# Kernel tuning notes

Hardware: AMD Instinct MI355X
Metric: run time of the kernel (lower is better)

Reference implementation:

```python
import jax, jax.numpy as jnp
from jax import lax
import numpy as np

T_NO = 50       # history / kernel half-length (hard-coded in module)
T_MAX = 101     # basis kernel length = 2*T_NO + 1
BASIS_NO = 34
HIST_BASIS_NO = 18
SIGMA = 3.0
HID = 20
SUB = 20


def _make_basis(n_basis, length):
    # basis[i, t] = exp(-(t - 3*i)^2 / sigma)
    raw = jnp.arange(length, dtype=jnp.float32)
    pts = 3.0 * jnp.arange(n_basis, dtype=jnp.float32)
    return jnp.exp(-((raw[None, :] - pts[:, None]) ** 2) / SIGMA)


def _conv1d(x, kern, pad):
    # x: [1, Cin, T], kern: [Cout, Cin, K] -> [1, Cout, T'] (torch F.conv1d semantics, cross-correlation)
    return lax.conv_general_dilated(x, kern, window_strides=(1,), padding=[(pad, pad)],
                                    dimension_numbers=('NCH', 'OIH', 'NCH'))


def setup_inputs() -> dict:
    key = jax.random.key(0)
    ks = jax.random.split(key, 12)
    T, Ee, Ei = 200000, 500, 100
    S_e = (jax.random.uniform(ks[0], (T, Ee)) < 0.05).astype(jnp.float32)
    S_i = (jax.random.uniform(ks[1], (T, Ei)) < 0.05).astype(jnp.float32)
    # one-hot synapse->subunit connectivity, as in the original model
    C_syn_e = jax.nn.one_hot(jax.random.randint(ks[2], (Ee,), 0, SUB), SUB, dtype=jnp.float32).T
    C_syn_i = jax.nn.one_hot(jax.random.randint(ks[3], (Ei,), 0, SUB), SUB, dtype=jnp.float32).T
    weight1 = 0.01 * jax.random.normal(ks[4], (HID, 2 * SUB, BASIS_NO), dtype=jnp.float32)
    weight4 = 0.01 * jax.random.normal(ks[5], (1, HID, BASIS_NO), dtype=jnp.float32)
    W_hist = 0.01 * jax.random.normal(ks[6], (HIST_BASIS_NO,), dtype=jnp.float32)
    Theta = 0.01 * jax.random.normal(ks[7], (1,), dtype=jnp.float32)
    W_spk = jnp.ones((1,), jnp.float32)
    Tau_spk = 3.0 * jnp.ones((1,), jnp.float32)
    u = jax.random.uniform(ks[8], (T,), dtype=jnp.float32)  # bernoulli noise
    return dict(S_e=S_e, S_i=S_i, C_syn_e=C_syn_e, C_syn_i=C_syn_i,
                weight1=weight1, weight4=weight4, W_hist=W_hist, Theta=Theta,
                W_spk=W_spk, Tau_spk=Tau_spk, u=u)


def reference(S_e, S_i, C_syn_e, C_syn_i, weight1, weight4, W_hist, Theta, W_spk, Tau_spk, u):
    basis = _make_basis(BASIS_NO, T_MAX)          # [34, 101]
    hist_basis = _make_basis(HIST_BASIS_NO, T_NO)  # [18, 50]

    kern1 = jnp.einsum('hsb,bt->hst', weight1, basis)  # [HID, 2*SUB, 101]
    kern4 = jnp.einsum('ohb,bt->oht', weight4, basis)  # [1, HID, 101]

    # route synapses to subunits, stack e/i: [1, 2*SUB, T]
    syn_in = jnp.concatenate([S_e @ C_syn_e.T, S_i @ C_syn_i.T], axis=1).T[None]
    out1 = jax.nn.leaky_relu(_conv1d(syn_in, kern1, T_NO), 0.01)  # [1, HID, T]
    out4 = _conv1d(out1, kern4, T_NO)[0, 0]                        # [T]

    hist_kern = W_hist @ hist_basis  # [50]
    theta = Theta[0]

    def step(buf, inp):
        # buf: last T_NO spikes, oldest first (== spk_out[t:t+T_NO])
        o_t, u_t = inp
        p = jax.nn.sigmoid(o_t + buf @ hist_kern + theta)
        spk = (u_t < p).astype(jnp.float32)  # torch.bernoulli(p)
        buf = jnp.concatenate([buf[1:], spk[None]])
        return buf, (p, spk)

    buf0 = jnp.zeros((T_NO,), jnp.float32)
    _, (prob_out, spikes) = lax.scan(step, buf0, (out4, u))
    spk_out = jnp.concatenate([jnp.zeros((T_NO,), jnp.float32), spikes])  # [T + T_NO]

    t = jnp.arange(T_NO, dtype=jnp.float32)
    t_tau = t / (Tau_spk[0] ** 2)
    spk_kern = t_tau * jnp.exp(-t_tau) * (W_spk[0] ** 2)  # unflipped; torch flips then cross-correlates
    # torch conv1d(x, flip(k), valid) == jnp.convolve(x, k, 'valid')
    spk_filt = jnp.convolve(spk_out, spk_kern, mode='valid')[:-1]  # [T]
    return (spk_filt, prob_out)
```

## Files before the change

kernel.cpp:

```cpp
#include <hip/hip_runtime.h>
#include <math.h>

#define T_TOT  200000
#define EE     500
#define EI     100
#define SUBN   20
#define NCH    40
#define HIDN   20
#define BNO    34
#define TM     101
#define TNO    50
#define HBNO   18
#define TT1    256
#define EPSF   2e-5f
#define NTAP   58

#define PADL   64
#define PADR   256
#define SROW   (PADL + T_TOT + PADR)

#define GROW   (T_TOT + 112)

#define GW     355
#define SW     380

#define RTILE  512
#define RHALO  64
#define RRND   3
#define NTILE  ((T_TOT + 1023) / 1024)

__global__ void k_setup(const float* __restrict__ Ce, const float* __restrict__ Ci,
                        const float* __restrict__ Wh, const float* __restrict__ Wspk,
                        const float* __restrict__ Tau,
                        int* __restrict__ ae, int* __restrict__ ai,
                        float* __restrict__ hkpos, float* __restrict__ hkneg,
                        float* __restrict__ spkk, float* __restrict__ gtap,
                        double* __restrict__ hkd, double* __restrict__ basisd)
{
    int tid = threadIdx.x;
    if (tid < EE) {
        int a = 0;
        for (int s = 0; s < SUBN; ++s) if (Ce[s * EE + tid] > 0.5f) a = s;
        ae[tid] = a;
    } else if (tid < EE + EI) {
        int e = tid - EE; int a = 0;
        for (int s = 0; s < SUBN; ++s) if (Ci[s * EI + e] > 0.5f) a = s;
        ai[e] = a;
    } else if (tid < 664) {
        int j = tid - 600;
        double hk = 0.0;
        if (j >= 1 && j <= TNO) {
            int i = TNO - j;
            for (int b = 0; b < HBNO; ++b) {
                double d = (double)i - 3.0 * (double)b;
                hk += (double)Wh[b] * exp(-d * d / 3.0);
            }
        }
        hkd[j] = hk;
        hkpos[j] = (float)fmax(hk, 0.0);
        hkneg[j] = (float)fmin(hk, 0.0);
    } else if (tid < 728) {
        int m = tid - 664; float v = 0.f;
        if (m < TNO) {
            double tau2 = (double)Tau[0] * (double)Tau[0];
            double tt = (double)m / tau2;
            v = (float)(tt * exp(-tt) * (double)Wspk[0] * (double)Wspk[0]);
        }
        spkk[m] = v;
    } else if (tid < 753) {
        int j = tid - 740;
        gtap[tid - 728] = (float)exp(-(double)(j * j) / 3.0);
    }
    for (int idx = tid; idx < BNO * TM; idx += blockDim.x) {
        int b = idx / TM, k = idx % TM;
        double d = (double)k - 3.0 * (double)b;
        basisd[idx] = exp(-d * d / 3.0);
    }
}

__global__ void k_prep(const float* __restrict__ w1, const float* __restrict__ w4,
                       const double* __restrict__ basisd,
                       float* __restrict__ kern4, float* __restrict__ cmerged,
                       float* __restrict__ syn)
{
    int idx = blockIdx.x * 256 + threadIdx.x;
    if (idx < HIDN * TM) {
        int h = idx % HIDN, k = idx / HIDN;
        double acc = 0.0;
        for (int b = 0; b < BNO; ++b) acc += (double)w4[h * BNO + b] * basisd[b * TM + k];
        kern4[k * HIDN + h] = (float)acc;
    } else if (idx < 2020 + NCH * NTAP * HIDN) {
        int j = idx - 2020;
        int h = j % HIDN, tap = (j / HIDN) % NTAP, s = j / (HIDN * NTAP);
        float val;
        if (tap < BNO) {
            val = w1[(h * NCH + s) * BNO + tap];
        } else {
            int mi = tap - BNO;
            int m = (mi < 12) ? (mi - 62) : (mi + 39);
            double acc = 0.0;
            for (int b = 0; b < BNO; ++b) {
                int jj = m + 50 - 3 * b;
                if (jj >= -12 && jj <= 12)
                    acc += (double)w1[(h * NCH + s) * BNO + b] * exp(-(double)(jj * jj) / 3.0);
            }
            val = -(float)acc;
        }
        cmerged[j] = val;
    } else if (idx < 2020 + NCH * NTAP * HIDN + NCH * (PADL + PADR)) {
        int j = idx - (2020 + NCH * NTAP * HIDN);
        int r = j / (PADL + PADR), c = j % (PADL + PADR);
        int off = (c < PADL) ? c : (PADL + T_TOT + (c - PADL));
        syn[(size_t)r * SROW + off] = 0.f;
    }
}

__global__ __launch_bounds__(256) void k_route(const float* __restrict__ Se,
                                               const float* __restrict__ Si,
                                               const int* __restrict__ ae,
                                               const int* __restrict__ ai,
                                               float* __restrict__ syn)
{
    __shared__ float acc[NCH * 64];
    __shared__ int sae[EE];
    __shared__ int sai[EI];
    int tid = threadIdx.x;
    for (int i = tid; i < NCH * 64; i += 256) acc[i] = 0.f;
    for (int i = tid; i < EE; i += 256) sae[i] = ae[i];
    for (int i = tid; i < EI; i += 256) sai[i] = ai[i];
    __syncthreads();
    int t0 = blockIdx.x * 64;
    int lane = tid & 63, grp = tid >> 6;
    for (int ec = 0; ec < 2; ++ec) {
        int ev = ec * 64 + lane;
        if (ev < EE / 4) {
            int e = 4 * ev;
            int a0 = sae[e], a1 = sae[e + 1], a2 = sae[e + 2], a3 = sae[e + 3];
            for (int ts = grp; ts < 64; ts += 8) {
                float4 v1 = *(const float4*)(Se + (size_t)(t0 + ts) * EE + e);
                float4 v2 = *(const float4*)(Se + (size_t)(t0 + ts + 4) * EE + e);
                if (v1.x != 0.f) atomicAdd(&acc[a0 * 64 + ts], v1.x);
                if (v1.y != 0.f) atomicAdd(&acc[a1 * 64 + ts], v1.y);
                if (v1.z != 0.f) atomicAdd(&acc[a2 * 64 + ts], v1.z);
                if (v1.w != 0.f) atomicAdd(&acc[a3 * 64 + ts], v1.w);
                if (v2.x != 0.f) atomicAdd(&acc[a0 * 64 + ts + 4], v2.x);
                if (v2.y != 0.f) atomicAdd(&acc[a1 * 64 + ts + 4], v2.y);
                if (v2.z != 0.f) atomicAdd(&acc[a2 * 64 + ts + 4], v2.z);
                if (v2.w != 0.f) atomicAdd(&acc[a3 * 64 + ts + 4], v2.w);
            }
        }
    }
    {
        int ev = lane;
        if (ev < EI / 4) {
            int e = 4 * ev;
            int a0 = sai[e] + SUBN, a1 = sai[e + 1] + SUBN, a2 = sai[e + 2] + SUBN, a3 = sai[e + 3] + SUBN;
            for (int ts = grp; ts < 64; ts += 8) {
                float4 v1 = *(const float4*)(Si + (size_t)(t0 + ts) * EI + e);
                float4 v2 = *(const float4*)(Si + (size_t)(t0 + ts + 4) * EI + e);
                if (v1.x != 0.f) atomicAdd(&acc[a0 * 64 + ts], v1.x);
                if (v1.y != 0.f) atomicAdd(&acc[a1 * 64 + ts], v1.y);
                if (v1.z != 0.f) atomicAdd(&acc[a2 * 64 + ts], v1.z);
                if (v1.w != 0.f) atomicAdd(&acc[a3 * 64 + ts], v1.w);
                if (v2.x != 0.f) atomicAdd(&acc[a0 * 64 + ts + 4], v2.x);
                if (v2.y != 0.f) atomicAdd(&acc[a1 * 64 + ts + 4], v2.y);
                if (v2.z != 0.f) atomicAdd(&acc[a2 * 64 + ts + 4], v2.z);
                if (v2.w != 0.f) atomicAdd(&acc[a3 * 64 + ts + 4], v2.w);
            }
        }
    }
    __syncthreads();
    for (int i = tid; i < NCH * 64; i += 256) {
        int s = i >> 6, ts = i & 63;
        syn[(size_t)s * SROW + PADL + t0 + ts] = acc[i];
    }
}

__global__ __launch_bounds__(256) void k_prefilt(const float* __restrict__ syn,
                                                 const float* __restrict__ gtap,
                                                 float* __restrict__ G)
{
    int gi = blockIdx.x * 256 + threadIdx.x;
    if (gi >= GROW) return;
    const float* sp = syn + (size_t)blockIdx.y * SROW + PADL + (gi - 50);
    double a = 0.0;
#pragma unroll
    for (int j = -12; j <= 12; ++j)
        a += (double)gtap[j + 12] * (double)sp[j];
    G[(size_t)blockIdx.y * GROW + gi] = (float)a;
}

__global__ __launch_bounds__(256) void k_conv1h(const float* __restrict__ G,
                                                const float* __restrict__ syn,
                                                const float* __restrict__ cmerged,
                                                float* __restrict__ out1)
{
    __shared__ float sg[2][GW];
    __shared__ float ss[2][SW];
    __shared__ float sc[2][NTAP * HIDN];
    int tid = threadIdx.x;
    int t0 = blockIdx.x * 256;
    int t = t0 + tid;

    {
        const float* Gp = G + t0;
        const float* sp = syn + PADL + t0 - 62;
        for (int i = tid; i < GW; i += 256)
            sg[0][i] = (t0 + i < GROW) ? Gp[i] : 0.f;
        for (int i = tid; i < SW; i += 256)
            ss[0][i] = sp[i];
        for (int i = tid; i < NTAP * HIDN; i += 256)
            sc[0][i] = cmerged[i];
    }

    float acc[HIDN];
#pragma unroll
    for (int h = 0; h < HIDN; ++h) acc[h] = 0.f;

    for (int s = 0; s < NCH; ++s) {
        __syncthreads();
        int cb = s & 1, nb = cb ^ 1;
        if (s + 1 < NCH) {
            const float* Gp = G + (size_t)(s + 1) * GROW + t0;
            const float* sp = syn + (size_t)(s + 1) * SROW + PADL + t0 - 62;
            const float* cp = cmerged + (size_t)(s + 1) * (NTAP * HIDN);
            for (int i = tid; i < GW; i += 256)
                sg[nb][i] = (t0 + i < GROW) ? Gp[i] : 0.f;
            for (int i = tid; i < SW; i += 256)
                ss[nb][i] = sp[i];
            for (int i = tid; i < NTAP * HIDN; i += 256)
                sc[nb][i] = cp[i];
        }
        const float* sgc = sg[cb];
        const float* ssc = ss[cb];
        const float* cc = sc[cb];
#pragma unroll 2
        for (int b = 0; b < BNO; ++b) {
            float gv = sgc[tid + 3 * b];
            const float4* cp4 = (const float4*)(cc + b * HIDN);
#pragma unroll
            for (int q = 0; q < 5; ++q) {
                float4 c = cp4[q];
                acc[4 * q + 0] = fmaf(c.x, gv, acc[4 * q + 0]);
                acc[4 * q + 1] = fmaf(c.y, gv, acc[4 * q + 1]);
                acc[4 * q + 2] = fmaf(c.z, gv, acc[4 * q + 2]);
                acc[4 * q + 3] = fmaf(c.w, gv, acc[4 * q + 3]);
            }
        }
#pragma unroll 2
        for (int mi = 0; mi < 12; ++mi) {
            float xv = ssc[tid + mi];
            const float4* cp4 = (const float4*)(cc + (BNO + mi) * HIDN);
#pragma unroll
            for (int q = 0; q < 5; ++q) {
                float4 c = cp4[q];
                acc[4 * q + 0] = fmaf(c.x, xv, acc[4 * q + 0]);
                acc[4 * q + 1] = fmaf(c.y, xv, acc[4 * q + 1]);
                acc[4 * q + 2] = fmaf(c.z, xv, acc[4 * q + 2]);
                acc[4 * q + 3] = fmaf(c.w, xv, acc[4 * q + 3]);
            }
        }
#pragma unroll 2
        for (int mi = 12; mi < 24; ++mi) {
            float xv = ssc[tid + mi + 101];
            const float4* cp4 = (const float4*)(cc + (BNO + mi) * HIDN);
#pragma unroll
            for (int q = 0; q < 5; ++q) {
                float4 c = cp4[q];
                acc[4 * q + 0] = fmaf(c.x, xv, acc[4 * q + 0]);
                acc[4 * q + 1] = fmaf(c.y, xv, acc[4 * q + 1]);
                acc[4 * q + 2] = fmaf(c.z, xv, acc[4 * q + 2]);
                acc[4 * q + 3] = fmaf(c.w, xv, acc[4 * q + 3]);
            }
        }
    }
    if (t < T_TOT) {
#pragma unroll
        for (int h = 0; h < HIDN; ++h) {
            float o = acc[h];
            out1[(size_t)h * T_TOT + t] = (o > 0.f) ? o : 0.01f * o;
        }
    }
}

__global__ __launch_bounds__(256) void k_conv2(const float* __restrict__ out1,
                                               const float* __restrict__ kern4,
                                               const float* __restrict__ Theta,
                                               const float* __restrict__ u,
                                               double* __restrict__ xd,
                                               double* __restrict__ thrd,
                                               float* __restrict__ thr32,
                                               float* __restrict__ blo,
                                               float* __restrict__ bhi)
{
    __shared__ float s1[HIDN * (TT1 + 100)];
    int tid = threadIdx.x;
    int t0 = blockIdx.x * TT1;
    for (int i = tid; i < HIDN * (TT1 + 100); i += 256) {
        int h = i / (TT1 + 100), x = i % (TT1 + 100);
        int g = t0 + x - TNO;
        s1[i] = (g >= 0 && g < T_TOT) ? out1[(size_t)h * T_TOT + g] : 0.f;
    }
    __syncthreads();
    int t = t0 + tid;
    if (t >= T_TOT) return;
    double acc = 0.0;
    for (int k = 0; k < TM; ++k) {
        const float* kp = kern4 + k * HIDN;
#pragma unroll
        for (int h = 0; h < HIDN; ++h)
            acc = fma((double)s1[h * (TT1 + 100) + tid + k], (double)kp[h], acc);
    }
    double x = acc + (double)Theta[0];
    double uu = (double)u[t];
    double th = (log(uu) - log1p(-uu)) - x;
    xd[t] = x; thrd[t] = th; thr32[t] = (float)th;
    blo[t + TNO] = 0.f;
    bhi[t + TNO] = 1.f;
    if (t < TNO) { blo[t] = 0.f; bhi[t] = 0.f; }
    if (t < 14)  { blo[T_TOT + TNO + t] = 0.f; bhi[T_TOT + TNO + t] = 0.f; }
}

__global__ __launch_bounds__(256) void k_relax(const float* __restrict__ thr32,
                                               const float* __restrict__ hkpos,
                                               const float* __restrict__ hkneg,
                                               float* __restrict__ blo,
                                               float* __restrict__ bhi)
{
    __shared__ float slo[RTILE + RHALO], shi[RTILE + RHALO];
    __shared__ float sth[RTILE + RHALO];
    __shared__ float shp[64], shn[64];
    int tid = threadIdx.x;
    int t0 = blockIdx.x * RTILE;
    for (int i = tid; i < RTILE + RHALO; i += 256) {
        int t = t0 - RHALO + i;
        int g = t + TNO;
        bool ok = (g >= 0 && g < T_TOT + 64);
        slo[i] = ok ? blo[g] : 0.f;
        shi[i] = ok ? bhi[g] : 0.f;
        sth[i] = (t >= 0 && t < T_TOT) ? thr32[t] : 0.f;
    }
    if (tid < 64) { shp[tid] = hkpos[tid]; shn[tid] = hkneg[tid]; }
    __syncthreads();
    for (int r = 0; r < RRND; ++r) {
        for (int i = tid; i < RTILE + RHALO; i += 256) {
            if (i < TNO) continue;
            float l = slo[i], h = shi[i];
            if (l == h) continue;
            float lo = 0.f, hi = 0.f;
            for (int j = 1; j <= TNO; ++j) {
                float bl = slo[i - j], bh = shi[i - j];
                float hp = shp[j], hn = shn[j];
                lo = fmaf(hp, bl, lo); lo = fmaf(hn, bh, lo);
                hi = fmaf(hp, bh, hi); hi = fmaf(hn, bl, hi);
            }
            float th = sth[i];
            if (lo > th + EPSF)      slo[i] = 1.f;
            else if (hi < th - EPSF) shi[i] = 0.f;
        }
        __syncthreads();
    }
    for (int i = tid; i < RTILE; i += 256) {
        int t = t0 + i;
        if (t < T_TOT) {
            blo[t + TNO] = slo[RHALO + i];
            bhi[t + TNO] = shi[RHALO + i];
        }
    }
}

__global__ __launch_bounds__(1024) void k_mark(const float* __restrict__ blo,
                                               const float* __restrict__ bhi,
                                               int* __restrict__ dirty)
{
    int t = blockIdx.x * 1024 + threadIdx.x;
    int unk = (t < T_TOT) && (blo[t + TNO] != bhi[t + TNO]);
    int c = __syncthreads_count(unk);
    if (threadIdx.x == 0) dirty[blockIdx.x] = c;
}

__global__ __launch_bounds__(1024) void k_compact(const float* __restrict__ blo,
                                                  const float* __restrict__ bhi,
                                                  const int* __restrict__ dirty,
                                                  int* __restrict__ list,
                                                  int* __restrict__ utot)
{
    __shared__ int wsum[16];
    __shared__ int sd[NTILE];
    __shared__ int sbase;
    int tid = threadIdx.x;
    if (tid < NTILE) sd[tid] = dirty[tid];
    int t = blockIdx.x * 1024 + tid;
    int unk = (t < T_TOT) && (blo[t + TNO] != bhi[t + TNO]);
    unsigned long long m = __ballot(unk);
    int lane = tid & 63, wv = tid >> 6;
    int lr = __popcll(m & ((1ull << lane) - 1ull));
    if (lane == 0) wsum[wv] = __popcll(m);
    __syncthreads();
    if (tid == 0) {
        int b = 0;
        for (int k = 0; k < (int)blockIdx.x; ++k) b += sd[k];
        sbase = b;
        if (blockIdx.x == 0) {
            int tot = 0;
            for (int k = 0; k < NTILE; ++k) tot += sd[k];
            utot[0] = tot;
        }
        int r = 0;
        for (int k = 0; k < 16; ++k) { int c = wsum[k]; wsum[k] = r; r += c; }
    }
    __syncthreads();
    if (unk) list[sbase + wsum[wv] + lr] = t;
}

__global__ __launch_bounds__(256) void k_afix(const int* __restrict__ list,
                                              const int* __restrict__ utot,
                                              const float* __restrict__ blo,
                                              const double* __restrict__ hkd,
                                              double* __restrict__ afix)
{
    int i = blockIdx.x * 256 + threadIdx.x;
    if (i >= utot[0]) return;
    int t = list[i];
    double a = 0.0;
    for (int j = 1; j <= TNO; ++j)
        a += hkd[j] * (double)blo[t - j + TNO];
    afix[i] = a;
}

__global__ __launch_bounds__(256) void k_chain(const int* __restrict__ list,
                                               int* __restrict__ utot,
                                               int* __restrict__ chead)
{
    __shared__ int wcnt[4];
    __shared__ int base_s;
    int tid = threadIdx.x, lane = tid & 63, wv = tid >> 6;
    int U = utot[0];
    if (tid == 0) base_s = 0;
    __syncthreads();
    for (int b0 = 0; b0 < U; b0 += 256) {
        int i = b0 + tid;
        int head = 0;
        if (i < U) head = (i == 0) || (list[i] - list[i - 1] > TNO);
        unsigned long long m = __ballot(head);
        int pre = __popcll(m & ((1ull << lane) - 1ull));
        if (lane == 0) wcnt[wv] = __popcll(m);
        __syncthreads();
        int wbase = 0;
        for (int k = 0; k < wv; ++k) wbase += wcnt[k];
        int tot = wcnt[0] + wcnt[1] + wcnt[2] + wcnt[3];
        if (head) chead[base_s + wbase + pre] = i;
        __syncthreads();
        if (tid == 0) base_s += tot;
        __syncthreads();
    }
    if (tid == 0) utot[1] = base_s;
}

__global__ __launch_bounds__(256) void k_cresolve(const int* __restrict__ list,
                                                  const int* __restrict__ chead,
                                                  const double* __restrict__ afix,
                                                  const double* __restrict__ thrd,
                                                  const double* __restrict__ hkd,
                                                  const int* __restrict__ utot,
                                                  int* bits,
                                                  float* __restrict__ blo,
                                                  float* __restrict__ bhi)
{
    __shared__ double shk[64];
    if (threadIdx.x < 64)
        shk[threadIdx.x] = (threadIdx.x >= 1 && threadIdx.x <= TNO) ? hkd[threadIdx.x] : 0.0;
    __syncthreads();
    int c = blockIdx.x * 256 + threadIdx.x;
    int nch = utot[1];
    if (c >= nch) return;
    int i0 = chead[c];
    int i1 = (c + 1 < nch) ? chead[c + 1] : utot[0];
    for (int i = i0; i < i1; ++i) {
        int t = list[i];
        double a = afix[i];
        for (int k = i - 1; k >= i0; --k) {
            int dt = t - list[k];
            if (dt > TNO) break;
            if (bits[k]) a += shk[dt];
        }
        int sb = (a > thrd[t]) ? 1 : 0;
        bits[i] = sb;
        float f = (float)sb;
        blo[t + TNO] = f;
        bhi[t + TNO] = f;
    }
}

__global__ __launch_bounds__(256) void k_out(const float* __restrict__ blo,
                                             const float* __restrict__ spkk,
                                             const double* __restrict__ hkd,
                                             const double* __restrict__ xd,
                                             float* __restrict__ outp)
{
    __shared__ float sb[TT1 + 64];
    __shared__ float ssp[64];
    __shared__ double shk[64];
    int tid = threadIdx.x;
    int t0 = blockIdx.x * TT1;
    for (int i = tid; i < TT1 + TNO; i += 256) {
        int g = t0 + i;
        sb[i] = (g < T_TOT + 64) ? blo[g] : 0.f;
    }
    if (tid < 64) { ssp[tid] = spkk[tid]; shk[tid] = hkd[tid]; }
    __syncthreads();
    int t = t0 + tid;
    if (t >= T_TOT) return;
    float filt = 0.f;
    double a = 0.0;
    for (int m = 1; m <= TNO; ++m) {
        float b = sb[tid + TNO - m];
        filt = fmaf(b, ssp[m - 1], filt);
        a += shk[m] * (double)b;
    }
    double p = 1.0 / (1.0 + exp(-(xd[t] + a)));
    outp[t] = filt;
    outp[T_TOT + t] = (float)p;
}

extern "C" void kernel_launch(void* const* d_in, const int* in_sizes, int n_in,
                              void* d_out, int out_size, void* d_ws, size_t ws_size,
                              hipStream_t stream)
{
    (void)in_sizes; (void)n_in; (void)out_size; (void)ws_size;
    const float* Se = (const float*)d_in[0];
    const float* Si = (const float*)d_in[1];
    const float* Ce = (const float*)d_in[2];
    const float* Ci = (const float*)d_in[3];
    const float* w1 = (const float*)d_in[4];
    const float* w4 = (const float*)d_in[5];
    const float* Wh = (const float*)d_in[6];
    const float* Th = (const float*)d_in[7];
    const float* Ws = (const float*)d_in[8];
    const float* Ta = (const float*)d_in[9];
    const float* u  = (const float*)d_in[10];

    char* w = (char*)d_ws;
    size_t off = 0;
    auto alloc = [&](size_t n) { size_t o = off; off += (n + 15) & ~(size_t)15; return o; };

    size_t gzone = alloc((size_t)NCH * GROW * 4);
    float*  G     = (float*)(w + gzone);
    double* xd    = (double*)(w + gzone);
    double* thrd  = (double*)(w + gzone + 1600000);
    float*  thr32 = (float*)(w + gzone + 3200000);
    float*  blo   = (float*)(w + gzone + 4000000);
    float*  bhi   = (float*)(w + gzone + 4800512);
    int*    dirty = (int*)(w + gzone + 5600768);
    int*    list  = (int*)(w + gzone + 5601792);
    double* afix  = (double*)(w + gzone + 6401792);
    int*    chead = (int*)(w + gzone + 8001792);
    int*    bits  = (int*)(w + gzone + 8801800);
    int*    utot  = dirty + 200;

    float*  syn     = (float*)(w + alloc((size_t)NCH * SROW * 4));
    float*  out1    = (float*)(w + alloc((size_t)HIDN * T_TOT * 4));
    float*  kern4   = (float*)(w + alloc((size_t)TM * HIDN * 4));
    float*  cmerged = (float*)(w + alloc((size_t)NCH * NTAP * HIDN * 4));
    double* basisd  = (double*)(w + alloc((size_t)BNO * TM * 8));
    int*    ae      = (int*)(w + alloc(EE * 4));
    int*    ai      = (int*)(w + alloc(EI * 4));
    float*  hkpos   = (float*)(w + alloc(64 * 4));
    float*  hkneg   = (float*)(w + alloc(64 * 4));
    float*  spkk    = (float*)(w + alloc(64 * 4));
    float*  gtap    = (float*)(w + alloc(32 * 4));
    double* hkd     = (double*)(w + alloc(64 * 8));

    k_setup<<<1, 1024, 0, stream>>>(Ce, Ci, Wh, Ws, Ta, ae, ai, hkpos, hkneg, spkk, gtap, hkd, basisd);
    int prepN = 2020 + NCH * NTAP * HIDN + NCH * (PADL + PADR);
    k_prep<<<(prepN + 255) / 256, 256, 0, stream>>>(w1, w4, basisd, kern4, cmerged, syn);
    k_route<<<T_TOT / 64, 256, 0, stream>>>(Se, Si, ae, ai, syn);
    dim3 pg((GROW + 255) / 256, NCH);
    k_prefilt<<<pg, 256, 0, stream>>>(syn, gtap, G);
    k_conv1h<<<(T_TOT + 255) / 256, 256, 0, stream>>>(G, syn, cmerged, out1);
    k_conv2<<<(T_TOT + TT1 - 1) / TT1, 256, 0, stream>>>(out1, kern4, Th, u, xd, thrd, thr32, blo, bhi);
    for (int r = 0; r < 4; ++r)
        k_relax<<<(T_TOT + RTILE - 1) / RTILE, 256, 0, stream>>>(thr32, hkpos, hkneg, blo, bhi);
    k_mark<<<NTILE, 1024, 0, stream>>>(blo, bhi, dirty);
    k_compact<<<NTILE, 1024, 0, stream>>>(blo, bhi, dirty, list, utot);
    k_chain<<<1, 256, 0, stream>>>(list, utot, chead);
    k_afix<<<(T_TOT + 255) / 256, 256, 0, stream>>>(list, utot, blo, hkd, afix);
    k_cresolve<<<(T_TOT + 255) / 256, 256, 0, stream>>>(list, chead, afix, thrd, hkd, utot, bits, blo, bhi);
    k_out<<<(T_TOT + TT1 - 1) / TT1, 256, 0, stream>>>(blo, spkk, hkd, xd, (float*)d_out);
}
```

Measured before the change: 1.195 ms.

## Register-block conv1 over two timesteps per thread and fuse dirty marking into relax

The first conv kernel now has each wave handle half of the hidden channels while each thread computes two adjacent timesteps. This halves the shared-memory coefficient loads per FMA, and the coefficients are repacked into a padded layout of 12 floats per tap. The relax pass count drops from four launches to two, with more rounds inside each launch. The separate mark kernel is replaced by a dirty-count written from the final relax. Compaction now uses 512-wide tiles to match, which cuts launches, but fewer relaxation passes may leave more unresolved timesteps for the later fixup stages.

```diff
diff --git a/kernel.cpp b/kernel.cpp
--- a/kernel.cpp
+++ b/kernel.cpp
@@ -14,6 +14,7 @@
 #define TT1    256
 #define EPSF   2e-5f
 #define NTAP   58
+#define CPT    12
 
 #define PADL   64
 #define PADR   256
@@ -23,11 +24,12 @@
 
 #define GW     355
 #define SW     380
+#define CW     (2 * NTAP * CPT)
 
 #define RTILE  512
 #define RHALO  64
-#define RRND   3
-#define NTILE  ((T_TOT + 1023) / 1024)
+#define RRND   4
+#define NT2    ((T_TOT + RTILE - 1) / RTILE)
 
 __global__ void k_setup(const float* __restrict__ Ce, const float* __restrict__ Ci,
                         const float* __restrict__ Wh, const float* __restrict__ Wspk,
@@ -89,26 +91,29 @@
         double acc = 0.0;
         for (int b = 0; b < BNO; ++b) acc += (double)w4[h * BNO + b] * basisd[b * TM + k];
         kern4[k * HIDN + h] = (float)acc;
-    } else if (idx < 2020 + NCH * NTAP * HIDN) {
+    } else if (idx < 2020 + NCH * CW) {
         int j = idx - 2020;
-        int h = j % HIDN, tap = (j / HIDN) % NTAP, s = j / (HIDN * NTAP);
-        float val;
-        if (tap < BNO) {
-            val = w1[(h * NCH + s) * BNO + tap];
-        } else {
-            int mi = tap - BNO;
-            int m = (mi < 12) ? (mi - 62) : (mi + 39);
-            double acc = 0.0;
-            for (int b = 0; b < BNO; ++b) {
-                int jj = m + 50 - 3 * b;
-                if (jj >= -12 && jj <= 12)
-                    acc += (double)w1[(h * NCH + s) * BNO + b] * exp(-(double)(jj * jj) / 3.0);
+        int f = j % CPT, tap = (j / CPT) % NTAP, hg = (j / (CPT * NTAP)) & 1, s = j / CW;
+        float val = 0.f;
+        if (f < 10) {
+            int h = hg * 10 + f;
+            if (tap < BNO) {
+                val = w1[(h * NCH + s) * BNO + tap];
+            } else {
+                int mi = tap - BNO;
+                int m = (mi < 12) ? (mi - 62) : (mi + 39);
+                double acc = 0.0;
+                for (int b = 0; b < BNO; ++b) {
+                    int jj = m + 50 - 3 * b;
+                    if (jj >= -12 && jj <= 12)
+                        acc += (double)w1[(h * NCH + s) * BNO + b] * exp(-(double)(jj * jj) / 3.0);
+                }
+                val = -(float)acc;
             }
-            val = -(float)acc;
         }
         cmerged[j] = val;
-    } else if (idx < 2020 + NCH * NTAP * HIDN + NCH * (PADL + PADR)) {
-        int j = idx - (2020 + NCH * NTAP * HIDN);
+    } else if (idx < 2020 + NCH * CW + NCH * (PADL + PADR)) {
+        int j = idx - (2020 + NCH * CW);
         int r = j / (PADL + PADR), c = j % (PADL + PADR);
         int off = (c < PADL) ? c : (PADL + T_TOT + (c - PADL));
         syn[(size_t)r * SROW + off] = 0.f;
@@ -190,32 +195,43 @@
     G[(size_t)blockIdx.y * GROW + gi] = (float)a;
 }
 
-__global__ __launch_bounds__(256) void k_conv1h(const float* __restrict__ G,
+#define FMA10(c0, c1, c2, v0, v1)                                              \
+    acc[0][0] = fmaf(c0.x, v0, acc[0][0]); acc[0][1] = fmaf(c0.x, v1, acc[0][1]); \
+    acc[1][0] = fmaf(c0.y, v0, acc[1][0]); acc[1][1] = fmaf(c0.y, v1, acc[1][1]); \
+    acc[2][0] = fmaf(c0.z, v0, acc[2][0]); acc[2][1] = fmaf(c0.z, v1, acc[2][1]); \
+    acc[3][0] = fmaf(c0.w, v0, acc[3][0]); acc[3][1] = fmaf(c0.w, v1, acc[3][1]); \
+    acc[4][0] = fmaf(c1.x, v0, acc[4][0]); acc[4][1] = fmaf(c1.x, v1, acc[4][1]); \
+    acc[5][0] = fmaf(c1.y, v0, acc[5][0]); acc[5][1] = fmaf(c1.y, v1, acc[5][1]); \
+    acc[6][0] = fmaf(c1.z, v0, acc[6][0]); acc[6][1] = fmaf(c1.z, v1, acc[6][1]); \
+    acc[7][0] = fmaf(c1.w, v0, acc[7][0]); acc[7][1] = fmaf(c1.w, v1, acc[7][1]); \
+    acc[8][0] = fmaf(c2.x, v0, acc[8][0]); acc[8][1] = fmaf(c2.x, v1, acc[8][1]); \
+    acc[9][0] = fmaf(c2.y, v0, acc[9][0]); acc[9][1] = fmaf(c2.y, v1, acc[9][1]);
+
+__global__ __launch_bounds__(256) void k_conv1w(const float* __restrict__ G,
                                                 const float* __restrict__ syn,
                                                 const float* __restrict__ cmerged,
                                                 float* __restrict__ out1)
 {
     __shared__ float sg[2][GW];
     __shared__ float ss[2][SW];
-    __shared__ float sc[2][NTAP * HIDN];
-    int tid = threadIdx.x;
+    __shared__ float sc[2][CW];
+    int tid = threadIdx.x;
+    int wv = tid >> 6, lane = tid & 63;
+    int hg = wv & 1, tsub = wv >> 1;
+    int tloc = tsub * 128 + lane * 2;
     int t0 = blockIdx.x * 256;
-    int t = t0 + tid;
 
     {
         const float* Gp = G + t0;
         const float* sp = syn + PADL + t0 - 62;
-        for (int i = tid; i < GW; i += 256)
-            sg[0][i] = (t0 + i < GROW) ? Gp[i] : 0.f;
-        for (int i = tid; i < SW; i += 256)
-            ss[0][i] = sp[i];
-        for (int i = tid; i < NTAP * HIDN; i += 256)
-            sc[0][i] = cmerged[i];
-    }
-
-    float acc[HIDN];
+        for (int i = tid; i < GW; i += 256) sg[0][i] = (t0 + i < GROW) ? Gp[i] : 0.f;
+        for (int i = tid; i < SW; i += 256) ss[0][i] = sp[i];
+        for (int i = tid; i < CW; i += 256) sc[0][i] = cmerged[i];
+    }
+
+    float acc[10][2];
 #pragma unroll
-    for (int h = 0; h < HIDN; ++h) acc[h] = 0.f;
+    for (int hh = 0; hh < 10; ++hh) { acc[hh][0] = 0.f; acc[hh][1] = 0.f; }
 
     for (int s = 0; s < NCH; ++s) {
         __syncthreads();
@@ -223,62 +239,51 @@
         if (s + 1 < NCH) {
             const float* Gp = G + (size_t)(s + 1) * GROW + t0;
             const float* sp = syn + (size_t)(s + 1) * SROW + PADL + t0 - 62;
-            const float* cp = cmerged + (size_t)(s + 1) * (NTAP * HIDN);
-            for (int i = tid; i < GW; i += 256)
-                sg[nb][i] = (t0 + i < GROW) ? Gp[i] : 0.f;
-            for (int i = tid; i < SW; i += 256)
-                ss[nb][i] = sp[i];
-            for (int i = tid; i < NTAP * HIDN; i += 256)
-                sc[nb][i] = cp[i];
-        }
-        const float* sgc = sg[cb];
-        const float* ssc = ss[cb];
-        const float* cc = sc[cb];
+            const float* cp = cmerged + (size_t)(s + 1) * CW;
+            for (int i = tid; i < GW; i += 256) sg[nb][i] = (t0 + i < GROW) ? Gp[i] : 0.f;
+            for (int i = tid; i < SW; i += 256) ss[nb][i] = sp[i];
+            for (int i = tid; i < CW; i += 256) sc[nb][i] = cp[i];
+        }
+        const float* sgc = sg[cb] + tloc;
+        const float* ssc = ss[cb] + tloc;
+        const float* cc = sc[cb] + hg * (NTAP * CPT);
 #pragma unroll 2
         for (int b = 0; b < BNO; ++b) {
-            float gv = sgc[tid + 3 * b];
-            const float4* cp4 = (const float4*)(cc + b * HIDN);
-#pragma unroll
-            for (int q = 0; q < 5; ++q) {
-                float4 c = cp4[q];
-                acc[4 * q + 0] = fmaf(c.x, gv, acc[4 * q + 0]);
-                acc[4 * q + 1] = fmaf(c.y, gv, acc[4 * q + 1]);
-                acc[4 * q + 2] = fmaf(c.z, gv, acc[4 * q + 2]);
-                acc[4 * q + 3] = fmaf(c.w, gv, acc[4 * q + 3]);
-            }
+            float v0 = sgc[3 * b], v1 = sgc[3 * b + 1];
+            const float* cp = cc + b * CPT;
+            float4 c0 = *(const float4*)cp;
+            float4 c1 = *(const float4*)(cp + 4);
+            float2 c2 = *(const float2*)(cp + 8);
+            FMA10(c0, c1, c2, v0, v1)
         }
 #pragma unroll 2
         for (int mi = 0; mi < 12; ++mi) {
-            float xv = ssc[tid + mi];
-            const float4* cp4 = (const float4*)(cc + (BNO + mi) * HIDN);
-#pragma unroll
-            for (int q = 0; q < 5; ++q) {
-                float4 c = cp4[q];
-                acc[4 * q + 0] = fmaf(c.x, xv, acc[4 * q + 0]);
-                acc[4 * q + 1] = fmaf(c.y, xv, acc[4 * q + 1]);
-                acc[4 * q + 2] = fmaf(c.z, xv, acc[4 * q + 2]);
-                acc[4 * q + 3] = fmaf(c.w, xv, acc[4 * q + 3]);
-            }
+            float v0 = ssc[mi], v1 = ssc[mi + 1];
+            const float* cp = cc + (BNO + mi) * CPT;
+            float4 c0 = *(const float4*)cp;
+            float4 c1 = *(const float4*)(cp + 4);
+            float2 c2 = *(const float2*)(cp + 8);
+            FMA10(c0, c1, c2, v0, v1)
         }
 #pragma unroll 2
         for (int mi = 12; mi < 24; ++mi) {
-            float xv = ssc[tid + mi + 101];
-            const float4* cp4 = (const float4*)(cc + (BNO + mi) * HIDN);
-#pragma unroll
-            for (int q = 0; q < 5; ++q) {
-                float4 c = cp4[q];
-                acc[4 * q + 0] = fmaf(c.x, xv, acc[4 * q + 0]);
-                acc[4 * q + 1] = fmaf(c.y, xv, acc[4 * q + 1]);
-                acc[4 * q + 2] = fmaf(c.z, xv, acc[4 * q + 2]);
-                acc[4 * q + 3] = fmaf(c.w, xv, acc[4 * q + 3]);
-            }
-        }
-    }
+            float v0 = ssc[mi + 101], v1 = ssc[mi + 102];
+            const float* cp = cc + (BNO + mi) * CPT;
+            float4 c0 = *(const float4*)cp;
+            float4 c1 = *(const float4*)(cp + 4);
+            float2 c2 = *(const float2*)(cp + 8);
+            FMA10(c0, c1, c2, v0, v1)
+        }
+    }
+    int t = t0 + tloc;
     if (t < T_TOT) {
 #pragma unroll
-        for (int h = 0; h < HIDN; ++h) {
-            float o = acc[h];
-            out1[(size_t)h * T_TOT + t] = (o > 0.f) ? o : 0.01f * o;
+        for (int hh = 0; hh < 10; ++hh) {
+            float o0 = acc[hh][0], o1 = acc[hh][1];
+            float2 st;
+            st.x = (o0 > 0.f) ? o0 : 0.01f * o0;
+            st.y = (o1 > 0.f) ? o1 : 0.01f * o1;
+            *(float2*)(out1 + (size_t)(hg * 10 + hh) * T_TOT + t) = st;
         }
     }
 }
@@ -325,7 +330,8 @@
                                                const float* __restrict__ hkpos,
                                                const float* __restrict__ hkneg,
                                                float* __restrict__ blo,
-                                               float* __restrict__ bhi)
+                                               float* __restrict__ bhi,
+                                               int wd, int* __restrict__ dirty)
 {
     __shared__ float slo[RTILE + RHALO], shi[RTILE + RHALO];
     __shared__ float sth[RTILE + RHALO];
@@ -367,30 +373,28 @@
             bhi[t + TNO] = shi[RHALO + i];
         }
     }
-}
-
-__global__ __launch_bounds__(1024) void k_mark(const float* __restrict__ blo,
-                                               const float* __restrict__ bhi,
-                                               int* __restrict__ dirty)
-{
-    int t = blockIdx.x * 1024 + threadIdx.x;
-    int unk = (t < T_TOT) && (blo[t + TNO] != bhi[t + TNO]);
-    int c = __syncthreads_count(unk);
-    if (threadIdx.x == 0) dirty[blockIdx.x] = c;
-}
-
-__global__ __launch_bounds__(1024) void k_compact(const float* __restrict__ blo,
-                                                  const float* __restrict__ bhi,
-                                                  const int* __restrict__ dirty,
-                                                  int* __restrict__ list,
-                                                  int* __restrict__ utot)
-{
-    __shared__ int wsum[16];
-    __shared__ int sd[NTILE];
+    if (wd) {
+        int i1 = tid, i2 = tid + 256;
+        int u1 = (t0 + i1 < T_TOT) && (slo[RHALO + i1] != shi[RHALO + i1]);
+        int u2 = (t0 + i2 < T_TOT) && (slo[RHALO + i2] != shi[RHALO + i2]);
+        int c = __syncthreads_count(u1);
+        c += __syncthreads_count(u2);
+        if (tid == 0) dirty[blockIdx.x] = c;
+    }
+}
+
+__global__ __launch_bounds__(512) void k_compact(const float* __restrict__ blo,
+                                                 const float* __restrict__ bhi,
+                                                 const int* __restrict__ dirty,
+                                                 int* __restrict__ list,
+                                                 int* __restrict__ utot)
+{
+    __shared__ int wsum[8];
+    __shared__ int sd[NT2];
     __shared__ int sbase;
     int tid = threadIdx.x;
-    if (tid < NTILE) sd[tid] = dirty[tid];
-    int t = blockIdx.x * 1024 + tid;
+    for (int i = tid; i < NT2; i += 512) sd[i] = dirty[i];
+    int t = blockIdx.x * 512 + tid;
     int unk = (t < T_TOT) && (blo[t + TNO] != bhi[t + TNO]);
     unsigned long long m = __ballot(unk);
     int lane = tid & 63, wv = tid >> 6;
@@ -403,11 +407,11 @@
         sbase = b;
         if (blockIdx.x == 0) {
             int tot = 0;
-            for (int k = 0; k < NTILE; ++k) tot += sd[k];
+            for (int k = 0; k < NT2; ++k) tot += sd[k];
             utot[0] = tot;
         }
         int r = 0;
-        for (int k = 0; k < 16; ++k) { int c = wsum[k]; wsum[k] = r; r += c; }
+        for (int k = 0; k < 8; ++k) { int c = wsum[k]; wsum[k] = r; r += c; }
     }
     __syncthreads();
     if (unk) list[sbase + wsum[wv] + lr] = t;
@@ -551,17 +555,17 @@
     float*  thr32 = (float*)(w + gzone + 3200000);
     float*  blo   = (float*)(w + gzone + 4000000);
     float*  bhi   = (float*)(w + gzone + 4800512);
-    int*    dirty = (int*)(w + gzone + 5600768);
-    int*    list  = (int*)(w + gzone + 5601792);
-    double* afix  = (double*)(w + gzone + 6401792);
-    int*    chead = (int*)(w + gzone + 8001792);
-    int*    bits  = (int*)(w + gzone + 8801800);
-    int*    utot  = dirty + 200;
+    int*    dirty = (int*)(w + gzone + 5601024);
+    int*    utot  = (int*)(w + gzone + 5603072);
+    int*    list  = (int*)(w + gzone + 5603200);
+    double* afix  = (double*)(w + gzone + 6403200);
+    int*    chead = (int*)(w + gzone + 8003200);
+    int*    bits  = (int*)(w + gzone + 8803216);
 
     float*  syn     = (float*)(w + alloc((size_t)NCH * SROW * 4));
     float*  out1    = (float*)(w + alloc((size_t)HIDN * T_TOT * 4));
     float*  kern4   = (float*)(w + alloc((size_t)TM * HIDN * 4));
-    float*  cmerged = (float*)(w + alloc((size_t)NCH * NTAP * HIDN * 4));
+    float*  cmerged = (float*)(w + alloc((size_t)NCH * CW * 4));
     double* basisd  = (double*)(w + alloc((size_t)BNO * TM * 8));
     int*    ae      = (int*)(w + alloc(EE * 4));
     int*    ai      = (int*)(w + alloc(EI * 4));
@@ -572,17 +576,16 @@
     double* hkd     = (double*)(w + alloc(64 * 8));
 
     k_setup<<<1, 1024, 0, stream>>>(Ce, Ci, Wh, Ws, Ta, ae, ai, hkpos, hkneg, spkk, gtap, hkd, basisd);
-    int prepN = 2020 + NCH * NTAP * HIDN + NCH * (PADL + PADR);
+    int prepN = 2020 + NCH * CW + NCH * (PADL + PADR);
     k_prep<<<(prepN + 255) / 256, 256, 0, stream>>>(w1, w4, basisd, kern4, cmerged, syn);
     k_route<<<T_TOT / 64, 256, 0, stream>>>(Se, Si, ae, ai, syn);
     dim3 pg((GROW + 255) / 256, NCH);
     k_prefilt<<<pg, 256, 0, stream>>>(syn, gtap, G);
-    k_conv1h<<<(T_TOT + 255) / 256, 256, 0, stream>>>(G, syn, cmerged, out1);
+    k_conv1w<<<(T_TOT + 255) / 256, 256, 0, stream>>>(G, syn, cmerged, out1);
     k_conv2<<<(T_TOT + TT1 - 1) / TT1, 256, 0, stream>>>(out1, kern4, Th, u, xd, thrd, thr32, blo, bhi);
-    for (int r = 0; r < 4; ++r)
-        k_relax<<<(T_TOT + RTILE - 1) / RTILE, 256, 0, stream>>>(thr32, hkpos, hkneg, blo, bhi);
-    k_mark<<<NTILE, 1024, 0, stream>>>(blo, bhi, dirty);
-    k_compact<<<NTILE, 1024, 0, stream>>>(blo, bhi, dirty, list, utot);
+    k_relax<<<NT2, 256, 0, stream>>>(thr32, hkpos, hkneg, blo, bhi, 0, dirty);
+    k_relax<<<NT2, 256, 0, stream>>>(thr32, hkpos, hkneg, blo, bhi, 1, dirty);
+    k_compact<<<NT2, 512, 0, stream>>>(blo, bhi, dirty, list, utot);
     k_chain<<<1, 256, 0, stream>>>(list, utot, chead);
     k_afix<<<(T_TOT + 255) / 256, 256, 0, stream>>>(list, utot, blo, hkd, afix);
     k_cresolve<<<(T_TOT + 255) / 256, 256, 0, stream>>>(list, chead, afix, thrd, hkd, utot, bits, blo, bhi);
```

Measured after the change: 1.133 ms. -5.2%, faster.
